# Kernel tuning notes

Hardware: AMD Instinct MI355X
Metric: run time of the kernel (lower is better)

## Reference

```python
import jax, jax.numpy as jnp
import numpy as np

B, S, H = 2, 2048, 2048
NH, NKV, HD = 16, 8, 128
EPS = 1e-6
THETA = 10000.0
SCALE = HD ** -0.5


def setup_inputs() -> dict:
    key = jax.random.key(0)
    ks = jax.random.split(key, 6)
    return {
        "positions": jnp.tile(jnp.arange(S, dtype=jnp.int64 if jax.config.jax_enable_x64 else jnp.int32), (B, 1)),
        "hidden_states": jax.random.normal(ks[0], (B, S, H), jnp.float32),
        "residual": jax.random.normal(ks[1], (B, S, H), jnp.float32),
        "layernorm_weight": 1.0 + 0.02 * jax.random.normal(ks[2], (H,), jnp.float32),
        "qkv_weight": 0.02 * jax.random.normal(ks[3], ((NH + 2 * NKV) * HD, H), jnp.float32),
        "o_weight": 0.02 * jax.random.normal(ks[4], (H, NH * HD), jnp.float32),
        "q_norm_weight": 1.0 + 0.02 * jax.random.normal(ks[5], (HD,), jnp.float32),
        "k_norm_weight": jnp.ones((HD,), jnp.float32),
    }


def _rmsnorm(x, w, eps=EPS):
    return x * jax.lax.rsqrt(jnp.mean(x * x, axis=-1, keepdims=True) + eps) * w


def _rope(x, positions):
    # x: [B, S, h, HD]; neox-style rotate-half RoPE
    inv_freq = 1.0 / (THETA ** (jnp.arange(0, HD, 2, dtype=jnp.float32) / HD))
    ang = positions.astype(jnp.float32)[..., None] * inv_freq  # [B, S, HD/2]
    cos = jnp.cos(ang)[:, :, None, :]
    sin = jnp.sin(ang)[:, :, None, :]
    x1, x2 = jnp.split(x, 2, axis=-1)
    return jnp.concatenate([x1 * cos - x2 * sin, x2 * cos + x1 * sin], axis=-1)


def reference(positions, hidden_states, residual, layernorm_weight,
              qkv_weight, o_weight, q_norm_weight, k_norm_weight):
    # Fused RMSNorm + QKV projection (on unnormalized hidden_states)
    xn = _rmsnorm(hidden_states, layernorm_weight)
    qkv = jnp.einsum('bsh,oh->bso', xn, qkv_weight)  # [B, S, (NH+2*NKV)*HD]
    q, k, v = jnp.split(qkv, [NH * HD, (NH + NKV) * HD], axis=-1)
    q = q.reshape(B, S, NH, HD)
    k = k.reshape(B, S, NKV, HD)
    v = v.reshape(B, S, NKV, HD)
    # per-head q/k RMSNorm (q_norm in fused QKV kernel, k_norm inside attention)
    q = _rmsnorm(q, q_norm_weight)
    k = _rmsnorm(k, k_norm_weight)
    # RoPE
    q = _rope(q, positions)
    k = _rope(k, positions)
    # GQA: expand KV heads
    rep = NH // NKV
    k = jnp.repeat(k, rep, axis=2)
    v = jnp.repeat(v, rep, axis=2)
    # causal attention
    scores = jnp.einsum('bqhd,bkhd->bhqk', q, k) * SCALE
    causal = jnp.tril(jnp.ones((S, S), bool))
    scores = jnp.where(causal[None, None], scores, jnp.finfo(scores.dtype).min)
    probs = jax.nn.softmax(scores, axis=-1)
    attn = jnp.einsum('bhqk,bkhd->bqhd', probs, v).reshape(B, S, NH * HD)
    # fused output projection + residual add
    return jnp.einsum('bsd,hd->bsh', attn, o_weight) + residual
```

## Files before the change

### kernel.cpp

```cpp
#include <hip/hip_runtime.h>
#include <hip/hip_bf16.h>

typedef __attribute__((ext_vector_type(8))) short bf16x8;
typedef __attribute__((ext_vector_type(4))) float f32x4;

#define B_ 2
#define S_ 2048
#define H_ 2048
#define NH_ 16
#define NKV_ 8
#define HD_ 128
#define M_ (B_ * S_)
#define NQKV_ ((NH_ + 2 * NKV_) * HD_)
#define QK_SCALE 0.08838834764831845f

#define VMCNT(n) asm volatile("s_waitcnt vmcnt(" #n ")" ::: "memory")

__device__ __forceinline__ unsigned short f2bf(float f) {
  unsigned int u = __float_as_uint(f);
  u += 0x7fffu + ((u >> 16) & 1u);
  return (unsigned short)(u >> 16);
}
__device__ __forceinline__ float bf2f(unsigned short h) {
  return __uint_as_float(((unsigned int)h) << 16);
}
__device__ __forceinline__ void gload_lds16(const void* g, void* l) {
  __builtin_amdgcn_global_load_lds(
      (const __attribute__((address_space(1))) void*)g,
      (__attribute__((address_space(3))) void*)l, 16, 0, 0);
}

__global__ __launch_bounds__(256) void k_rmsnorm(
    const float* __restrict__ x, const float* __restrict__ w,
    unsigned short* __restrict__ out) {
  __shared__ float red[4];
  const int m = blockIdx.x;
  const int t = threadIdx.x;
  const float4* row = (const float4*)(x + (size_t)m * H_);
  float4 v0 = row[t];
  float4 v1 = row[t + 256];
  float ss = v0.x * v0.x + v0.y * v0.y + v0.z * v0.z + v0.w * v0.w +
             v1.x * v1.x + v1.y * v1.y + v1.z * v1.z + v1.w * v1.w;
#pragma unroll
  for (int mk = 1; mk < 64; mk <<= 1) ss += __shfl_xor(ss, mk);
  if ((t & 63) == 0) red[t >> 6] = ss;
  __syncthreads();
  ss = red[0] + red[1] + red[2] + red[3];
  const float sc = rsqrtf(ss * (1.0f / H_) + 1e-6f);
  const float4* wv = (const float4*)w;
  float4 w0 = wv[t], w1 = wv[t + 256];
  ushort4 o0, o1;
  o0.x = f2bf(v0.x * sc * w0.x);
  o0.y = f2bf(v0.y * sc * w0.y);
  o0.z = f2bf(v0.z * sc * w0.z);
  o0.w = f2bf(v0.w * sc * w0.w);
  o1.x = f2bf(v1.x * sc * w1.x);
  o1.y = f2bf(v1.y * sc * w1.y);
  o1.z = f2bf(v1.z * sc * w1.z);
  o1.w = f2bf(v1.w * sc * w1.w);
  ushort4* orow = (ushort4*)(out + (size_t)m * H_);
  orow[t] = o0;
  orow[t + 256] = o1;
}

__global__ __launch_bounds__(256) void k_f32_to_bf16(
    const float* __restrict__ in, unsigned short* __restrict__ out, int n4) {
  int idx = blockIdx.x * 256 + threadIdx.x;
  const int stride = gridDim.x * 256;
  for (; idx < n4; idx += stride) {
    float4 v = ((const float4*)in)[idx];
    ushort4 o;
    o.x = f2bf(v.x);
    o.y = f2bf(v.y);
    o.z = f2bf(v.z);
    o.w = f2bf(v.w);
    ((ushort4*)out)[idx] = o;
  }
}

__global__ __launch_bounds__(256) void k_rope_table(
    const int* __restrict__ positions, float* __restrict__ cos_t,
    float* __restrict__ sin_t) {
  int idx = blockIdx.x * 256 + threadIdx.x;
  if (idx >= B_ * S_ * 64) return;
  int d = idx & 63;
  int bs = idx >> 6;
  float pos = (float)positions[bs];
  float inv_freq = powf(10000.0f, -(float)(2 * d) * (1.0f / HD_));
  float ang = pos * inv_freq;
  cos_t[idx] = cosf(ang);
  sin_t[idx] = sinf(ang);
}

template <int FMB>
__device__ __forceinline__ void load_a256(const unsigned short* sAb, int wm,
                                          int lr, int lg, bf16x8 (&af)[2][4]) {
#pragma unroll
  for (int kk = 0; kk < 2; ++kk) {
    const int pc = kk * 4 + lg;
#pragma unroll
    for (int i = 0; i < 4; ++i) {
      const int R = wm + (FMB + i) * 16 + lr;
      const int idx = ((R >> 6) & 1) * 8192 +
                      ((((R >> 7) << 6) | (R & 63)) << 6) +
                      ((pc ^ (R & 7)) << 3);
      af[kk][i] = *(const bf16x8*)&sAb[idx];
    }
  }
}
template <int FNB>
__device__ __forceinline__ void load_b256(const unsigned short* sBb, int wn,
                                          int lr, int lg, bf16x8 (&bfv)[2][2]) {
#pragma unroll
  for (int kk = 0; kk < 2; ++kk) {
    const int pc = kk * 4 + lg;
#pragma unroll
    for (int j = 0; j < 2; ++j) {
      const int R = wn + (FNB + j) * 16 + lr;
      const int idx = ((R >> 5) & 1) * 8192 +
                      ((((R >> 6) << 5) | (R & 31)) << 6) +
                      ((pc ^ (R & 7)) << 3);
      bfv[kk][j] = *(const bf16x8*)&sBb[idx];
    }
  }
}

template <int FMB, int FNB>
__device__ __forceinline__ void phase_mfma(const bf16x8 (&af)[2][4],
                                           const bf16x8 (&bfv)[2][2],
                                           f32x4 (&acc)[8][4]) {
#pragma unroll
  for (int kk = 0; kk < 2; ++kk)
#pragma unroll
    for (int i = 0; i < 4; ++i)
#pragma unroll
      for (int j = 0; j < 2; ++j)
        acc[FMB + i][FNB + j] = __builtin_amdgcn_mfma_f32_16x16x32_bf16(
            af[kk][i], bfv[kk][j], acc[FMB + i][FNB + j], 0, 0, 0);
}

__global__ __launch_bounds__(512, 2) void k_gemm256(
    const unsigned short* __restrict__ A, const unsigned short* __restrict__ Bt,
    unsigned short* __restrict__ C, int M, int N, int K) {
  __shared__ unsigned short sA[2][256 * 64];
  __shared__ unsigned short sB[2][256 * 64];
  const int tid = threadIdx.x;
  const int w = tid >> 6;
  const int l = tid & 63;
  const int lr = l & 15, lg = l >> 4;
  const int gx = gridDim.x;
  const int lin = blockIdx.y * gx + blockIdx.x;
  const int cpx = (gx * gridDim.y) >> 3;
  const int swz = (lin & 7) * cpx + (lin >> 3);
  const int m0 = (swz / gx) * 256, n0 = (swz % gx) * 256;
  const int wm = (w >> 2) * 128, wn = (w & 3) * 64;
  f32x4 acc[8][4] = {};

  auto stageA = [&](int t, int bufi, int h) {
    const int k0 = t * 64;
#pragma unroll
    for (int i = 0; i < 2; ++i) {
      const int L = i * 512 + tid;
      const int r = L >> 3;
      const int R = ((r >> 6) << 7) | (h << 6) | (r & 63);
      const int d = (L & 7) ^ (r & 7);
      gload_lds16(A + (size_t)(m0 + R) * K + k0 + d * 8,
                  (char*)sA[bufi] + h * 16384 +
                      (size_t)(i * 512 + w * 64) * 16);
    }
  };
  auto stageB = [&](int t, int bufi, int h) {
    const int k0 = t * 64;
#pragma unroll
    for (int i = 0; i < 2; ++i) {
      const int L = i * 512 + tid;
      const int r = L >> 3;
      const int R = ((r >> 5) << 6) | (h << 5) | (r & 31);
      const int d = (L & 7) ^ (r & 7);
      gload_lds16(Bt + (size_t)(n0 + R) * K + k0 + d * 8,
                  (char*)sB[bufi] + h * 16384 +
                      (size_t)(i * 512 + w * 64) * 16);
    }
  };

#define PH_TAIL()                                      \
  __builtin_amdgcn_s_barrier();                        \
  asm volatile("s_waitcnt lgkmcnt(0)" ::: "memory");   \
  __builtin_amdgcn_sched_barrier(0)

  stageA(0, 0, 0);
  stageB(0, 0, 0);
  stageA(0, 0, 1);
  stageB(0, 0, 1);
  VMCNT(0);
  __builtin_amdgcn_s_barrier();
  __builtin_amdgcn_sched_barrier(0);

  bf16x8 af[2][4];
  bf16x8 bfv[2][2];
  const int NT = K >> 6;
  for (int t = 0; t < NT; ++t) {
    const int bufi = t & 1;
    const int nb = bufi ^ 1;
    const bool st = (t + 1 < NT);
    load_a256<0>(sA[bufi], wm, lr, lg, af);
    load_b256<0>(sB[bufi], wn, lr, lg, bfv);
    if (st) stageA(t + 1, nb, 0);
    PH_TAIL();
    __builtin_amdgcn_s_setprio(1);
    phase_mfma<0, 0>(af, bfv, acc);
    __builtin_amdgcn_s_setprio(0);
    if (st) {
      VMCNT(4);
    } else {
      VMCNT(2);
    }
    __builtin_amdgcn_s_barrier();
    __builtin_amdgcn_sched_barrier(0);
    load_a256<4>(sA[bufi], wm, lr, lg, af);
    if (st) stageB(t + 1, nb, 0);
    PH_TAIL();
    __builtin_amdgcn_s_setprio(1);
    phase_mfma<4, 0>(af, bfv, acc);
    __builtin_amdgcn_s_setprio(0);
    if (st) {
      VMCNT(4);
    } else {
      VMCNT(0);
    }
    __builtin_amdgcn_s_barrier();
    __builtin_amdgcn_sched_barrier(0);
    load_b256<2>(sB[bufi], wn, lr, lg, bfv);
    if (st) stageA(t + 1, nb, 1);
    PH_TAIL();
    __builtin_amdgcn_s_setprio(1);
    phase_mfma<4, 2>(af, bfv, acc);
    __builtin_amdgcn_s_setprio(0);
    __builtin_amdgcn_s_barrier();
    __builtin_amdgcn_sched_barrier(0);
    load_a256<0>(sA[bufi], wm, lr, lg, af);
    if (st) stageB(t + 1, nb, 1);
    PH_TAIL();
    __builtin_amdgcn_s_setprio(1);
    phase_mfma<0, 2>(af, bfv, acc);
    __builtin_amdgcn_s_setprio(0);
    if (st) VMCNT(4);
    __builtin_amdgcn_s_barrier();
    __builtin_amdgcn_sched_barrier(0);
  }
#undef PH_TAIL

#pragma unroll
  for (int fm = 0; fm < 8; ++fm)
#pragma unroll
    for (int fn = 0; fn < 4; ++fn)
#pragma unroll
      for (int r = 0; r < 4; ++r) {
        const int row = m0 + wm + fm * 16 + lg * 4 + r;
        const int col = n0 + wn + fn * 16 + lr;
        C[(size_t)row * N + col] = f2bf(acc[fm][fn][r]);
      }
}

template <int FMB>
__device__ __forceinline__ void load_ao(const unsigned short* sAb, int wm,
                                        int lr, int lg, bf16x8 (&af)[2][2]) {
#pragma unroll
  for (int kk = 0; kk < 2; ++kk) {
    const int pc = kk * 4 + lg;
#pragma unroll
    for (int i = 0; i < 2; ++i) {
      const int R = wm + (FMB + i) * 16 + lr;
      const int idx = ((R >> 5) & 1) * 8192 +
                      ((((R >> 6) << 5) | (R & 31)) << 6) +
                      ((pc ^ (R & 7)) << 3);
      af[kk][i] = *(const bf16x8*)&sAb[idx];
    }
  }
}
template <int FNB>
__device__ __forceinline__ void load_bo(const unsigned short* sBb, int wn,
                                        int lr, int lg, bf16x8 (&bfv)[2][2]) {
#pragma unroll
  for (int kk = 0; kk < 2; ++kk) {
    const int pc = kk * 4 + lg;
#pragma unroll
    for (int j = 0; j < 2; ++j) {
      const int R = wn + (FNB + j) * 16 + lr;
      const int idx = ((R >> 5) & 1) * 4096 +
                      ((((R >> 6) << 5) | (R & 31)) << 6) +
                      ((pc ^ (R & 7)) << 3);
      bfv[kk][j] = *(const bf16x8*)&sBb[idx];
    }
  }
}

template <int FMB, int FNB>
__device__ __forceinline__ void phase_mfma_o(const bf16x8 (&af)[2][2],
                                             const bf16x8 (&bfv)[2][2],
                                             f32x4 (&acc)[4][4]) {
#pragma unroll
  for (int kk = 0; kk < 2; ++kk)
#pragma unroll
    for (int i = 0; i < 2; ++i)
#pragma unroll
      for (int j = 0; j < 2; ++j)
        acc[FMB + i][FNB + j] = __builtin_amdgcn_mfma_f32_16x16x32_bf16(
            af[kk][i], bfv[kk][j], acc[FMB + i][FNB + j], 0, 0, 0);
}

__global__ __launch_bounds__(512, 1) void k_gemm_ores(
    const unsigned short* __restrict__ A, const unsigned short* __restrict__ Bt,
    float* __restrict__ Cout, const float* __restrict__ resid, int M, int N,
    int K) {
  __shared__ unsigned short sA[2][256 * 64];
  __shared__ unsigned short sB[2][128 * 64];
  const int tid = threadIdx.x;
  const int w = tid >> 6;
  const int l = tid & 63;
  const int lr = l & 15, lg = l >> 4;
  const int gx = gridDim.x;
  const int lin = blockIdx.y * gx + blockIdx.x;
  const int cpx = (gx * gridDim.y) >> 3;
  const int swz = (lin & 7) * cpx + (lin >> 3);
  const int m0 = (swz / gx) * 256, n0 = (swz % gx) * 128;
  const int wm = (w >> 1) * 64, wn = (w & 1) * 64;
  f32x4 acc[4][4] = {};

  auto stageAo = [&](int t, int bufi, int h) {
    const int k0 = t * 64;
#pragma unroll
    for (int i = 0; i < 2; ++i) {
      const int L = i * 512 + tid;
      const int r = L >> 3;
      const int R = ((r >> 5) << 6) | (h << 5) | (r & 31);
      const int d = (L & 7) ^ (r & 7);
      gload_lds16(A + (size_t)(m0 + R) * K + k0 + d * 8,
                  (char*)sA[bufi] + h * 16384 +
                      (size_t)(i * 512 + w * 64) * 16);
    }
  };
  auto stageBo = [&](int t, int bufi, int h) {
    const int k0 = t * 64;
    const int L = tid;
    const int r = L >> 3;
    const int R = ((r >> 5) << 6) | (h << 5) | (r & 31);
    const int d = (L & 7) ^ (r & 7);
    gload_lds16(Bt + (size_t)(n0 + R) * K + k0 + d * 8,
                (char*)sB[bufi] + h * 8192 + (size_t)(w * 64) * 16);
  };

#define PH_TAIL()                                      \
  __builtin_amdgcn_s_barrier();                        \
  asm volatile("s_waitcnt lgkmcnt(0)" ::: "memory");   \
  __builtin_amdgcn_sched_barrier(0)

  stageAo(0, 0, 0);
  stageBo(0, 0, 0);
  stageAo(0, 0, 1);
  stageBo(0, 0, 1);
  VMCNT(0);
  __builtin_amdgcn_s_barrier();
  __builtin_amdgcn_sched_barrier(0);

  bf16x8 af[2][2];
  bf16x8 bfv[2][2];
  const int NT = K >> 6;
  for (int t = 0; t < NT; ++t) {
    const int bufi = t & 1;
    const int nb = bufi ^ 1;
    const bool st = (t + 1 < NT);
    load_ao<0>(sA[bufi], wm, lr, lg, af);
    load_bo<0>(sB[bufi], wn, lr, lg, bfv);
    if (st) stageAo(t + 1, nb, 0);
    PH_TAIL();
    __builtin_amdgcn_s_setprio(1);
    phase_mfma_o<0, 0>(af, bfv, acc);
    __builtin_amdgcn_s_setprio(0);
    if (st) {
      VMCNT(3);
    } else {
      VMCNT(1);
    }
    __builtin_amdgcn_s_barrier();
    __builtin_amdgcn_sched_barrier(0);
    load_ao<2>(sA[bufi], wm, lr, lg, af);
    if (st) stageBo(t + 1, nb, 0);
    PH_TAIL();
    __builtin_amdgcn_s_setprio(1);
    phase_mfma_o<2, 0>(af, bfv, acc);
    __builtin_amdgcn_s_setprio(0);
    if (st) {
      VMCNT(3);
    } else {
      VMCNT(0);
    }
    __builtin_amdgcn_s_barrier();
    __builtin_amdgcn_sched_barrier(0);
    load_bo<2>(sB[bufi], wn, lr, lg, bfv);
    if (st) stageAo(t + 1, nb, 1);
    PH_TAIL();
    __builtin_amdgcn_s_setprio(1);
    phase_mfma_o<2, 2>(af, bfv, acc);
    __builtin_amdgcn_s_setprio(0);
    __builtin_amdgcn_s_barrier();
    __builtin_amdgcn_sched_barrier(0);
    load_ao<0>(sA[bufi], wm, lr, lg, af);
    if (st) stageBo(t + 1, nb, 1);
    PH_TAIL();
    __builtin_amdgcn_s_setprio(1);
    phase_mfma_o<0, 2>(af, bfv, acc);
    __builtin_amdgcn_s_setprio(0);
    if (st) VMCNT(3);
    __builtin_amdgcn_s_barrier();
    __builtin_amdgcn_sched_barrier(0);
  }
#undef PH_TAIL

#pragma unroll
  for (int i = 0; i < 4; ++i)
#pragma unroll
    for (int j = 0; j < 4; ++j)
#pragma unroll
      for (int r = 0; r < 4; ++r) {
        const int row = m0 + wm + i * 16 + lg * 4 + r;
        const int col = n0 + wn + j * 16 + lr;
        const size_t o = (size_t)row * N + col;
        Cout[o] = acc[i][j][r] + resid[o];
      }
}

__global__ __launch_bounds__(256) void k_postprocess(
    const unsigned short* __restrict__ qkv, const float* __restrict__ qw,
    const float* __restrict__ kw, const float* __restrict__ cos_t,
    const float* __restrict__ sin_t, unsigned short* __restrict__ qb,
    unsigned short* __restrict__ kb, unsigned short* __restrict__ vb) {
  const int m = blockIdx.x;
  const int b = m >> 11, s = m & (S_ - 1);
  const int w = threadIdx.x >> 6, l = threadIdx.x & 63;
  const unsigned short* row = qkv + (size_t)m * NQKV_;
  const float c = cos_t[(size_t)m * 64 + l];
  const float sn = sin_t[(size_t)m * 64 + l];
  for (int hh = w * 8; hh < w * 8 + 8; ++hh) {
    int base, type;
    unsigned short* out;
    const float* nw;
    if (hh < NH_) {
      type = 0;
      base = hh * HD_;
      out = qb + ((size_t)(b * NH_ + hh) * S_ + s) * HD_;
      nw = qw;
    } else if (hh < NH_ + NKV_) {
      int kh = hh - NH_;
      type = 1;
      base = NH_ * HD_ + kh * HD_;
      out = kb + ((size_t)(b * NKV_ + kh) * S_ + s) * HD_;
      nw = kw;
    } else {
      int kh = hh - NH_ - NKV_;
      type = 2;
      base = (NH_ + NKV_) * HD_ + kh * HD_;
      out = vb + ((size_t)(b * NKV_ + kh) * S_ + s) * HD_;
      nw = nullptr;
    }
    unsigned short r1 = row[base + l];
    unsigned short r2 = row[base + 64 + l];
    if (type == 2) {
      out[l] = r1;
      out[64 + l] = r2;
      continue;
    }
    float x1 = bf2f(r1), x2 = bf2f(r2);
    float ss = x1 * x1 + x2 * x2;
#pragma unroll
    for (int mk = 1; mk < 64; mk <<= 1) ss += __shfl_xor(ss, mk);
    float sc = rsqrtf(ss * (1.0f / HD_) + 1e-6f);
    float y1 = x1 * sc * nw[l];
    float y2 = x2 * sc * nw[64 + l];
    float o1 = y1 * c - y2 * sn;
    float o2 = y2 * c + y1 * sn;
    if (type == 0) {
      o1 *= QK_SCALE;
      o2 *= QK_SCALE;
    }
    out[l] = f2bf(o1);
    out[64 + l] = f2bf(o2);
  }
}

__global__ __launch_bounds__(256) void k_transpose_v(
    const unsigned short* __restrict__ in,
    unsigned short* __restrict__ out) {
  __shared__ unsigned short tile[32][33];
  const int bx = blockIdx.x, by = blockIdx.y, bz = blockIdx.z;
  const unsigned short* src = in + (size_t)bz * S_ * HD_;
  unsigned short* dst = out + (size_t)bz * S_ * HD_;
  const int tx = threadIdx.x & 31, ty = threadIdx.x >> 5;
#pragma unroll
  for (int i = ty; i < 32; i += 8)
    tile[i][tx] = src[(size_t)(bx * 32 + i) * HD_ + by * 32 + tx];
  __syncthreads();
#pragma unroll
  for (int i = ty; i < 32; i += 8)
    dst[(size_t)(by * 32 + i) * S_ + bx * 32 + tx] = tile[tx][i];
}

#define MFIX 13.0f
__global__ __launch_bounds__(512, 4) void k_attn(
    const unsigned short* __restrict__ Q,
    const unsigned short* __restrict__ K,
    const unsigned short* __restrict__ VT,
    unsigned short* __restrict__ Oa) {
  __shared__ unsigned short kt[2][64 * 128];
  __shared__ unsigned short vt[2][128 * 64];
  __shared__ unsigned short pls[8 * 16 * 64];
  const int bh = blockIdx.y;
  const int b = bh >> 4, h = bh & 15;
  const int kvh = b * NKV_ + (h >> 1);
  const int xa = blockIdx.x;
  const int xb = 31 - xa;
  const int tid = threadIdx.x;
  const int w = tid >> 6, l = tid & 63;
  const int lr = l & 15, lg = l >> 4;
  const int wr = (w & 3) * 16;
  const int myx = (w < 4) ? xa : xb;
  const int q0m = myx * 64;

  bf16x8 qf[4];
  {
    const unsigned short* Qp = Q + ((size_t)bh * S_ + q0m + wr) * HD_;
#pragma unroll
    for (int tt = 0; tt < 4; ++tt)
      qf[tt] = *(const bf16x8*)(Qp + (size_t)lr * HD_ + tt * 32 + lg * 8);
  }
  f32x4 ao[8] = {};
  float lrow[4] = {0.f, 0.f, 0.f, 0.f};
  const unsigned short* Kp = K + (size_t)kvh * S_ * HD_;
  const unsigned short* Vp = VT + (size_t)kvh * HD_ * S_;
  unsigned short* pw = pls + w * 1024;

  auto stage = [&](int t, int bufi) {
    const int k0 = t * 64;
#pragma unroll
    for (int i = 0; i < 2; ++i) {
      const int chunk = i * 512 + tid;
      {
        const int r = chunk >> 4, p = chunk & 15;
        const int d = p ^ (r & 7);
        gload_lds16(Kp + (size_t)(k0 + r) * HD_ + d * 8,
                    (char*)kt[bufi] + (size_t)(i * 512 + w * 64) * 16);
      }
      {
        const int r = chunk >> 3, p = chunk & 7;
        const int d = p ^ (r & 7);
        gload_lds16(Vp + (size_t)r * S_ + k0 + d * 8,
                    (char*)vt[bufi] + (size_t)(i * 512 + w * 64) * 16);
      }
    }
  };

  auto process = [&](int t, int bufi, bool diag) {
    const unsigned short* ktb = kt[bufi];
    const unsigned short* vtb = vt[bufi];
    f32x4 sc[4] = {};
#pragma unroll
    for (int j = 0; j < 4; ++j)
#pragma unroll
      for (int tt = 0; tt < 4; ++tt) {
        bf16x8 kf = *(const bf16x8*)&ktb[(j * 16 + lr) * 128 +
                                         (((tt * 4 + lg) ^ (lr & 7)) << 3)];
        sc[j] =
            __builtin_amdgcn_mfma_f32_16x16x32_bf16(qf[tt], kf, sc[j], 0, 0, 0);
      }
    if (diag) {
      const int kvc = t * 64 + lr;
      const int qg = q0m + wr + lg * 4;
#pragma unroll
      for (int j = 0; j < 4; ++j)
#pragma unroll
        for (int r = 0; r < 4; ++r)
          if (kvc + j * 16 > qg + r) sc[j][r] = -1e30f;
    }
#pragma unroll
    for (int j = 0; j < 4; ++j)
#pragma unroll
      for (int r = 0; r < 4; ++r) {
        float p = __expf(sc[j][r] - MFIX);
        lrow[r] += p;
        const int row = lg * 4 + r;
        const int pchunk = ((j * 2) + (lr >> 3)) ^ (row & 7);
        pw[row * 64 + pchunk * 8 + (lr & 7)] = f2bf(p);
      }
#pragma unroll
    for (int ks = 0; ks < 2; ++ks) {
      bf16x8 pf =
          *(const bf16x8*)&pw[lr * 64 + (((ks * 4 + lg) ^ (lr & 7)) << 3)];
#pragma unroll
      for (int dj = 0; dj < 8; ++dj) {
        bf16x8 vf = *(const bf16x8*)&vtb[(dj * 16 + lr) * 64 +
                                         (((ks * 4 + lg) ^ (lr & 7)) << 3)];
        ao[dj] =
            __builtin_amdgcn_mfma_f32_16x16x32_bf16(pf, vf, ao[dj], 0, 0, 0);
      }
    }
  };

  stage(0, 0);
  __syncthreads();
  int cur = 0;
  for (int t = 0; t <= xb; ++t) {
    if (t < xb) stage(t + 1, cur ^ 1);
    if (t <= myx) process(t, cur, t == myx);
    __syncthreads();
    cur ^= 1;
  }

  float inv[4];
#pragma unroll
  for (int r = 0; r < 4; ++r) {
#pragma unroll
    for (int mk = 1; mk < 16; mk <<= 1) lrow[r] += __shfl_xor(lrow[r], mk);
    inv[r] = 1.0f / lrow[r];
  }
#pragma unroll
  for (int dj = 0; dj < 8; ++dj)
#pragma unroll
    for (int r = 0; r < 4; ++r) {
      const int sg = q0m + wr + lg * 4 + r;
      const size_t o =
          ((size_t)b * S_ + sg) * (NH_ * HD_) + h * HD_ + dj * 16 + lr;
      Oa[o] = f2bf(ao[dj][r] * inv[r]);
    }
}

extern "C" void kernel_launch(void* const* d_in, const int* in_sizes, int n_in,
                              void* d_out, int out_size, void* d_ws,
                              size_t ws_size, hipStream_t stream) {
  const int* positions = (const int*)d_in[0];
  const float* hidden = (const float*)d_in[1];
  const float* residual = (const float*)d_in[2];
  const float* ln_w = (const float*)d_in[3];
  const float* qkv_w = (const float*)d_in[4];
  const float* o_w = (const float*)d_in[5];
  const float* q_nw = (const float*)d_in[6];
  const float* k_nw = (const float*)d_in[7];

  char* ws = (char*)d_ws;
  const size_t SZ_XN = (size_t)M_ * H_ * 2;
  const size_t SZ_QKVW = (size_t)NQKV_ * H_ * 2;
  const size_t SZ_OW = (size_t)H_ * (NH_ * HD_) * 2;
  const size_t SZ_QKV = (size_t)M_ * NQKV_ * 2;
  const size_t SZ_KB = (size_t)B_ * NKV_ * S_ * HD_ * 2;
  const size_t SZ_COS = (size_t)B_ * S_ * 64 * 4;

  unsigned short* xn = (unsigned short*)(ws);
  unsigned short* q_buf = (unsigned short*)(ws);
  unsigned short* qkvw_bf = (unsigned short*)(ws + SZ_XN);
  unsigned short* k_buf = (unsigned short*)(ws + SZ_XN);
  unsigned short* v_buf = (unsigned short*)(ws + SZ_XN + SZ_KB);
  unsigned short* owbf = (unsigned short*)(ws + SZ_XN + SZ_QKVW);
  unsigned short* qkv_bf = (unsigned short*)(ws + SZ_XN + SZ_QKVW + SZ_OW);
  unsigned short* attn_o = qkv_bf;
  unsigned short* vt_buf =
      (unsigned short*)(ws + SZ_XN + SZ_QKVW + SZ_OW + SZ_QKV);
  float* cos_t = (float*)(ws + SZ_XN + SZ_QKVW + SZ_OW + SZ_QKV + SZ_KB);
  float* sin_t = (float*)((char*)cos_t + SZ_COS);

  k_rmsnorm<<<M_, 256, 0, stream>>>(hidden, ln_w, xn);
  k_f32_to_bf16<<<2048, 256, 0, stream>>>(qkv_w, qkvw_bf,
                                          (int)(SZ_QKVW / 2 / 4));
  k_f32_to_bf16<<<1024, 256, 0, stream>>>(o_w, owbf, (int)(SZ_OW / 2 / 4));
  k_rope_table<<<(B_ * S_ * 64) / 256, 256, 0, stream>>>(positions, cos_t,
                                                         sin_t);
  k_gemm256<<<dim3(NQKV_ / 256, M_ / 256), 512, 0, stream>>>(
      xn, qkvw_bf, qkv_bf, M_, NQKV_, H_);
  k_postprocess<<<M_, 256, 0, stream>>>(qkv_bf, q_nw, k_nw, cos_t, sin_t,
                                        q_buf, k_buf, v_buf);
  k_transpose_v<<<dim3(S_ / 32, HD_ / 32, B_ * NKV_), 256, 0, stream>>>(v_buf,
                                                                        vt_buf);
  k_attn<<<dim3(16, B_ * NH_), 512, 0, stream>>>(q_buf, k_buf, vt_buf, attn_o);
  k_gemm_ores<<<dim3((NH_ * HD_) / 128, M_ / 256), 512, 0, stream>>>(
      attn_o, owbf, (float*)d_out, residual, M_, NH_ * HD_, H_);
}
```

Baseline: 241.8 us.

## Collapse GEMM k-loop to two phases with double B fragments; add setprio in attention

Both GEMM kernels (QKV and output projection) now run two barrier-separated phases per k-tile instead of four. Both B fragment halves are held in separate registers, so A is reloaded only once per tile. Global-to-LDS staging is regrouped to match, with adjusted vmcnt waits, including a partial wait in the prologue. This cuts barriers and LDS reloads per tile at the cost of more registers and larger MFMA bursts. The attention kernel also gets s_setprio around its MFMA blocks to favor matrix issue across waves.

```diff
diff --git a/kernel.cpp b/kernel.cpp
--- a/kernel.cpp
+++ b/kernel.cpp
@@ -183,72 +183,61 @@
     }
   };
 
-#define PH_TAIL()                                      \
-  __builtin_amdgcn_s_barrier();                        \
+#define BARR()                          \
+  __builtin_amdgcn_s_barrier();         \
+  __builtin_amdgcn_sched_barrier(0)
+#define LGKM0()                                        \
   asm volatile("s_waitcnt lgkmcnt(0)" ::: "memory");   \
   __builtin_amdgcn_sched_barrier(0)
 
   stageA(0, 0, 0);
   stageB(0, 0, 0);
+  stageB(0, 0, 1);
   stageA(0, 0, 1);
-  stageB(0, 0, 1);
-  VMCNT(0);
-  __builtin_amdgcn_s_barrier();
-  __builtin_amdgcn_sched_barrier(0);
+  VMCNT(2);
+  BARR();
 
   bf16x8 af[2][4];
-  bf16x8 bfv[2][2];
+  bf16x8 bfv0[2][2];
+  bf16x8 bfv1[2][2];
   const int NT = K >> 6;
   for (int t = 0; t < NT; ++t) {
     const int bufi = t & 1;
     const int nb = bufi ^ 1;
     const bool st = (t + 1 < NT);
     load_a256<0>(sA[bufi], wm, lr, lg, af);
-    load_b256<0>(sB[bufi], wn, lr, lg, bfv);
-    if (st) stageA(t + 1, nb, 0);
-    PH_TAIL();
+    load_b256<0>(sB[bufi], wn, lr, lg, bfv0);
+    load_b256<2>(sB[bufi], wn, lr, lg, bfv1);
+    if (st) {
+      stageA(t + 1, nb, 0);
+      stageB(t + 1, nb, 0);
+    }
+    __builtin_amdgcn_s_barrier();
+    LGKM0();
     __builtin_amdgcn_s_setprio(1);
-    phase_mfma<0, 0>(af, bfv, acc);
-    __builtin_amdgcn_s_setprio(0);
-    if (st) {
-      VMCNT(4);
-    } else {
-      VMCNT(2);
-    }
-    __builtin_amdgcn_s_barrier();
-    __builtin_amdgcn_sched_barrier(0);
-    load_a256<4>(sA[bufi], wm, lr, lg, af);
-    if (st) stageB(t + 1, nb, 0);
-    PH_TAIL();
-    __builtin_amdgcn_s_setprio(1);
-    phase_mfma<4, 0>(af, bfv, acc);
+    phase_mfma<0, 0>(af, bfv0, acc);
+    phase_mfma<0, 2>(af, bfv1, acc);
     __builtin_amdgcn_s_setprio(0);
     if (st) {
       VMCNT(4);
     } else {
       VMCNT(0);
     }
+    BARR();
+    load_a256<4>(sA[bufi], wm, lr, lg, af);
+    if (st) {
+      stageB(t + 1, nb, 1);
+      stageA(t + 1, nb, 1);
+    }
     __builtin_amdgcn_s_barrier();
-    __builtin_amdgcn_sched_barrier(0);
-    load_b256<2>(sB[bufi], wn, lr, lg, bfv);
-    if (st) stageA(t + 1, nb, 1);
-    PH_TAIL();
+    LGKM0();
     __builtin_amdgcn_s_setprio(1);
-    phase_mfma<4, 2>(af, bfv, acc);
+    phase_mfma<4, 2>(af, bfv1, acc);
+    phase_mfma<4, 0>(af, bfv0, acc);
     __builtin_amdgcn_s_setprio(0);
-    __builtin_amdgcn_s_barrier();
-    __builtin_amdgcn_sched_barrier(0);
-    load_a256<0>(sA[bufi], wm, lr, lg, af);
-    if (st) stageB(t + 1, nb, 1);
-    PH_TAIL();
-    __builtin_amdgcn_s_setprio(1);
-    phase_mfma<0, 2>(af, bfv, acc);
-    __builtin_amdgcn_s_setprio(0);
-    if (st) VMCNT(4);
-    __builtin_amdgcn_s_barrier();
-    __builtin_amdgcn_sched_barrier(0);
-  }
-#undef PH_TAIL
+    if (st) VMCNT(2);
+    BARR();
+  }
 
 #pragma unroll
   for (int fm = 0; fm < 8; ++fm)
@@ -260,6 +249,8 @@
         const int col = n0 + wn + fn * 16 + lr;
         C[(size_t)row * N + col] = f2bf(acc[fm][fn][r]);
       }
+#undef BARR
+#undef LGKM0
 }
 
 template <int FMB>
@@ -350,72 +341,61 @@
                 (char*)sB[bufi] + h * 8192 + (size_t)(w * 64) * 16);
   };
 
-#define PH_TAIL()                                      \
-  __builtin_amdgcn_s_barrier();                        \
+#define BARR()                          \
+  __builtin_amdgcn_s_barrier();         \
+  __builtin_amdgcn_sched_barrier(0)
+#define LGKM0()                                        \
   asm volatile("s_waitcnt lgkmcnt(0)" ::: "memory");   \
   __builtin_amdgcn_sched_barrier(0)
 
   stageAo(0, 0, 0);
   stageBo(0, 0, 0);
+  stageBo(0, 0, 1);
   stageAo(0, 0, 1);
-  stageBo(0, 0, 1);
-  VMCNT(0);
-  __builtin_amdgcn_s_barrier();
-  __builtin_amdgcn_sched_barrier(0);
+  VMCNT(2);
+  BARR();
 
   bf16x8 af[2][2];
-  bf16x8 bfv[2][2];
+  bf16x8 bfv0[2][2];
+  bf16x8 bfv1[2][2];
   const int NT = K >> 6;
   for (int t = 0; t < NT; ++t) {
     const int bufi = t & 1;
     const int nb = bufi ^ 1;
     const bool st = (t + 1 < NT);
     load_ao<0>(sA[bufi], wm, lr, lg, af);
-    load_bo<0>(sB[bufi], wn, lr, lg, bfv);
-    if (st) stageAo(t + 1, nb, 0);
-    PH_TAIL();
+    load_bo<0>(sB[bufi], wn, lr, lg, bfv0);
+    load_bo<2>(sB[bufi], wn, lr, lg, bfv1);
+    if (st) {
+      stageAo(t + 1, nb, 0);
+      stageBo(t + 1, nb, 0);
+    }
+    __builtin_amdgcn_s_barrier();
+    LGKM0();
     __builtin_amdgcn_s_setprio(1);
-    phase_mfma_o<0, 0>(af, bfv, acc);
-    __builtin_amdgcn_s_setprio(0);
-    if (st) {
-      VMCNT(3);
-    } else {
-      VMCNT(1);
-    }
-    __builtin_amdgcn_s_barrier();
-    __builtin_amdgcn_sched_barrier(0);
-    load_ao<2>(sA[bufi], wm, lr, lg, af);
-    if (st) stageBo(t + 1, nb, 0);
-    PH_TAIL();
-    __builtin_amdgcn_s_setprio(1);
-    phase_mfma_o<2, 0>(af, bfv, acc);
+    phase_mfma_o<0, 0>(af, bfv0, acc);
+    phase_mfma_o<0, 2>(af, bfv1, acc);
     __builtin_amdgcn_s_setprio(0);
     if (st) {
       VMCNT(3);
     } else {
       VMCNT(0);
     }
+    BARR();
+    load_ao<2>(sA[bufi], wm, lr, lg, af);
+    if (st) {
+      stageBo(t + 1, nb, 1);
+      stageAo(t + 1, nb, 1);
+    }
     __builtin_amdgcn_s_barrier();
-    __builtin_amdgcn_sched_barrier(0);
-    load_bo<2>(sB[bufi], wn, lr, lg, bfv);
-    if (st) stageAo(t + 1, nb, 1);
-    PH_TAIL();
+    LGKM0();
     __builtin_amdgcn_s_setprio(1);
-    phase_mfma_o<2, 2>(af, bfv, acc);
+    phase_mfma_o<2, 2>(af, bfv1, acc);
+    phase_mfma_o<2, 0>(af, bfv0, acc);
     __builtin_amdgcn_s_setprio(0);
-    __builtin_amdgcn_s_barrier();
-    __builtin_amdgcn_sched_barrier(0);
-    load_ao<0>(sA[bufi], wm, lr, lg, af);
-    if (st) stageBo(t + 1, nb, 1);
-    PH_TAIL();
-    __builtin_amdgcn_s_setprio(1);
-    phase_mfma_o<0, 2>(af, bfv, acc);
-    __builtin_amdgcn_s_setprio(0);
-    if (st) VMCNT(3);
-    __builtin_amdgcn_s_barrier();
-    __builtin_amdgcn_sched_barrier(0);
-  }
-#undef PH_TAIL
+    if (st) VMCNT(2);
+    BARR();
+  }
 
 #pragma unroll
   for (int i = 0; i < 4; ++i)
@@ -428,6 +408,8 @@
         const size_t o = (size_t)row * N + col;
         Cout[o] = acc[i][j][r] + resid[o];
       }
+#undef BARR
+#undef LGKM0
 }
 
 __global__ __launch_bounds__(256) void k_postprocess(
@@ -563,6 +545,7 @@
     const unsigned short* ktb = kt[bufi];
     const unsigned short* vtb = vt[bufi];
     f32x4 sc[4] = {};
+    __builtin_amdgcn_s_setprio(1);
 #pragma unroll
     for (int j = 0; j < 4; ++j)
 #pragma unroll
@@ -572,6 +555,7 @@
         sc[j] =
             __builtin_amdgcn_mfma_f32_16x16x32_bf16(qf[tt], kf, sc[j], 0, 0, 0);
       }
+    __builtin_amdgcn_s_setprio(0);
     if (diag) {
       const int kvc = t * 64 + lr;
       const int qg = q0m + wr + lg * 4;
@@ -591,6 +575,7 @@
         const int pchunk = ((j * 2) + (lr >> 3)) ^ (row & 7);
         pw[row * 64 + pchunk * 8 + (lr & 7)] = f2bf(p);
       }
+    __builtin_amdgcn_s_setprio(1);
 #pragma unroll
     for (int ks = 0; ks < 2; ++ks) {
       bf16x8 pf =
@@ -603,6 +588,7 @@
             __builtin_amdgcn_mfma_f32_16x16x32_bf16(pf, vf, ao[dj], 0, 0, 0);
       }
     }
+    __builtin_amdgcn_s_setprio(0);
   };
 
   stage(0, 0);
```

Result: faster. 224.3 us (-7.2%).
